# Kernel tuning notes

Measured on AMD Instinct MI355X. Metric: run time of the kernel, lower is better.

Reference implementation:

```python
import jax, jax.numpy as jnp
import numpy as np

DIM = 48
HF = int(DIM * 2.66)  # 127 hidden_features

_DN = ('NCHW', 'OIHW', 'NCHW')

def _gconv3(x, w, groups):
    # 3x3 grouped conv, stride 1, zero pad 1 (torch Conv2d default padding)
    return jax.lax.conv_general_dilated(x, w, (1, 1), [(1, 1), (1, 1)],
                                         dimension_numbers=_DN,
                                         feature_group_count=groups)

def _g1x1(x, w):
    # grouped 1x1 conv; w: (groups, out_per_group, in_per_group)
    B, C, H, W = x.shape
    g = w.shape[0]
    xr = x.reshape(B, g, C // g, H, W)
    y = jnp.einsum('bgihw,goi->bgohw', xr, w)
    return y.reshape(B, g * w.shape[1], H, W)

def _shuffle(x):
    # channel shuffle with 4 groups (reshape/permute as in the torch module)
    B, C, H, W = x.shape
    return x.reshape(B, C // 4, 4, H * W).transpose(0, 2, 1, 3).reshape(B, C, H, W)

def _avgconv(x):
    # frozen dense 3x3 conv with all weights 1/9 and replicate padding:
    # every output channel equals box_blur(sum over input channels) / 9
    s = jnp.sum(x, axis=1, keepdims=True) * jnp.asarray(1.0 / 9.0, x.dtype)
    sp = jnp.pad(s, ((0, 0), (0, 0), (1, 1), (1, 1)), mode='edge')
    k = jnp.ones((1, 1, 3, 3), x.dtype)
    b = jax.lax.conv_general_dilated(sp, k, (1, 1), 'VALID', dimension_numbers=_DN)
    return jnp.broadcast_to(b, x.shape)

def setup_inputs() -> dict:
    key = jax.random.key(0)
    ks = jax.random.split(key, 10)
    s = 0.05
    return {
        'x':     jax.random.normal(ks[0], (2, DIM, 256, 256), jnp.float32),
        'w_inP': jax.random.normal(ks[1], (2 * HF, DIM), jnp.float32) * s,
        'w_inD': jax.random.normal(ks[2], (4 * HF, 1, 3, 3), jnp.float32) * s,
        'w_lp1': jax.random.normal(ks[3], (HF, 4, 4), jnp.float32) * s,
        'w_hp1': jax.random.normal(ks[4], (HF, 4, 4), jnp.float32) * s,
        'w_lp2': jax.random.normal(ks[5], (HF, 4, 4), jnp.float32) * s,
        'w_hp2': jax.random.normal(ks[6], (HF, 4, 4), jnp.float32) * s,
        'w_ld':  jax.random.normal(ks[7], (HF, 4, 3, 3), jnp.float32) * s,
        'w_hd':  jax.random.normal(ks[8], (HF, 4, 3, 3), jnp.float32) * s,
        'w_out': jax.random.normal(ks[9], (DIM, 2 * HF), jnp.float32) * s,
    }

def reference(x, w_inP, w_inD, w_lp1, w_hp1, w_lp2, w_hp2, w_ld, w_hd, w_out):
    residual = x
    # inPconv (dense 1x1) -> inDconv (groups=2h, multiplier 2) -> ReLU
    t = jnp.einsum('bchw,oc->bohw', x, w_inP)            # (B, 2h, H, W)
    t = jax.nn.relu(_gconv3(t, w_inD, 2 * HF))            # (B, 4h, H, W)
    l = _avgconv(t)
    h = t - l
    l = jax.nn.relu(_g1x1(l, w_lp1))
    h = jax.nn.relu(_g1x1(h, w_hp1))
    l = _shuffle(l)
    h = _shuffle(h)
    l2 = _g1x1(l, w_lp2)
    h2 = _g1x1(h, w_hp2)
    c = 2 * HF
    l_tol, l_toh = l2[:, :c], l2[:, c:]
    h_toh, h_tol = h2[:, :c], h2[:, c:]
    l = jax.nn.relu(_gconv3(jnp.concatenate([l_tol, h_tol], axis=1), w_ld, HF))
    h = jax.nn.relu(_gconv3(jnp.concatenate([h_toh, l_toh], axis=1), w_hd, HF))
    out = jnp.einsum('bchw,oc->bohw', jnp.concatenate([l, h], axis=1), w_out)
    return out + residual
```

## Files before the change

kernel.cpp:

```cpp
#include <hip/hip_runtime.h>
#include <hip/hip_bf16.h>

#define HW 65536
#define NCH 16

typedef __attribute__((ext_vector_type(8))) short bf16x8;
typedef __attribute__((ext_vector_type(4))) float f32x4;
typedef __attribute__((ext_vector_type(2))) float f32x2;
typedef __attribute__((ext_vector_type(2))) short s16x2;

__device__ __forceinline__ float bfu(unsigned short u){
    return __uint_as_float(((unsigned int)u) << 16);
}
__device__ __forceinline__ float bflo(unsigned int u){
    return __uint_as_float(u << 16);
}
__device__ __forceinline__ float bfhi(unsigned int u){
    return __uint_as_float(u & 0xffff0000u);
}
__device__ __forceinline__ unsigned short f2bu(float f){
    return __builtin_bit_cast(unsigned short, __float2bfloat16(f));
}
__device__ __forceinline__ unsigned int pk2(float a, float b){
    return (unsigned int)f2bu(a) | ((unsigned int)f2bu(b) << 16);
}
__device__ __forceinline__ unsigned int pk2c(float a, float b){
    unsigned int r;
    asm("v_cvt_pk_bf16_f32 %0, %1, %2" : "=v"(r) : "v"(a), "v"(b));
    return r;
}

#if __has_builtin(__builtin_amdgcn_fdot2_f32_bf16)
__device__ __forceinline__ float DOT2B(s16x2 a, s16x2 b, float c){
    return __builtin_amdgcn_fdot2_f32_bf16(a, b, c, false);
}
#else
__device__ __forceinline__ float DOT2B(s16x2 a, s16x2 b, float c){
    return fmaf(bfu((unsigned short)a.x), bfu((unsigned short)b.x),
           fmaf(bfu((unsigned short)a.y), bfu((unsigned short)b.y), c));
}
#endif

__global__ void k_coef1(const float* __restrict__ wlp1, const float* __restrict__ whp1,
                        const float* __restrict__ wlp2,
                        float* __restrict__ ahp1s,
                        float* __restrict__ cpG, float* __restrict__ cnG){
    __shared__ float aL[508], ah[508];
    int t = threadIdx.x;
    if (t < 508){
        int g = t >> 2, o = t & 3;
        float s = 0.f, s2 = 0.f;
        for (int i = 0; i < 4; ++i){ s += wlp1[g*16 + o*4 + i]; s2 += whp1[g*16 + o*4 + i]; }
        aL[t] = s; ah[t] = s2;
    }
    __syncthreads();
    if (t < 508){
        int g = t >> 2, o = t & 3;
        float p = 0.f, n = 0.f;
        for (int k = 0; k < 4; ++k){
            int idx = 4*g + k;
            int inv = (idx % 127)*4 + idx/127;
            float av = aL[inv];
            float w2 = wlp2[g*16 + o*4 + k];
            p += w2 * fmaxf(av, 0.f);
            n += w2 * fminf(av, 0.f);
        }
        cpG[t] = p; cnG[t] = n;
        int inv = (t % 127)*4 + t/127;
        ahp1s[t] = ah[inv];
    }
}

__global__ void k_coef2(const float* __restrict__ wld, const float* __restrict__ whd,
                        const float* __restrict__ winP, const float* __restrict__ winD,
                        const float* __restrict__ wout,
                        const float* __restrict__ cp, const float* __restrict__ cn,
                        unsigned int* __restrict__ WPNL, unsigned int* __restrict__ WPNH,
                        unsigned int* __restrict__ WLDpk, unsigned int* __restrict__ WHDpk,
                        float* __restrict__ wDp,
                        unsigned short* __restrict__ WPb, unsigned short* __restrict__ BtP){
    int t0 = blockIdx.x*256 + threadIdx.x;
    int str = gridDim.x*256;
    for (int idx = t0; idx < 127*9; idx += str){
        int g = idx/9, q = idx%9;
        float lp=0.f, ln=0.f, hp=0.f, hn=0.f;
        for (int i = 0; i < 4; ++i){
            int ch = 4*g + i;
            if (ch < 254){ float w = wld[g*36 + i*9 + q]; lp += w*cp[ch]; ln += w*cn[ch]; }
            else         { float w = whd[g*36 + i*9 + q]; hp += w*cp[ch]; hn += w*cn[ch]; }
        }
        WPNL[idx] = pk2(lp, ln);
        WPNH[idx] = pk2(hp, hn);
    }
    for (int idx = t0; idx < 127*18; idx += str){
        int g = idx/18, r = idx%18; int q = r >> 1, hp_ = r & 1;
        int c0 = 4*g + 2*hp_, c1 = c0 + 1;
        float wl0 = (c0 >= 254) ? wld[g*36 + (2*hp_)*9 + q]   : 0.f;
        float wl1 = (c1 >= 254) ? wld[g*36 + (2*hp_+1)*9 + q] : 0.f;
        float wh0 = (c0 <  254) ? whd[g*36 + (2*hp_)*9 + q]   : 0.f;
        float wh1 = (c1 <  254) ? whd[g*36 + (2*hp_+1)*9 + q] : 0.f;
        WLDpk[idx] = pk2(wl0, wl1);
        WHDpk[idx] = pk2(wh0, wh1);
    }
    for (int idx = t0; idx < 512*9; idx += str){
        int ch = idx/9, q = idx - ch*9;
        wDp[idx] = (ch < 508) ? winD[ch*9 + q] : 0.f;
    }
    for (int idx = t0; idx < 256*64; idx += str){
        int o = idx >> 6, k = idx & 63;
        float vv = (o < 254 && k < 48) ? winP[o*48 + k] : 0.f;
        WPb[idx] = f2bu(vv);
    }
    for (int idx = t0; idx < 48*256; idx += str){
        int n = idx >> 8, k = idx & 255;
        int g = k >> 1;
        float vv = (g < 127) ? ((k & 1) ? wout[n*254 + 127 + g] : wout[n*254 + g]) : 0.f;
        BtP[idx] = f2bu(vv);
    }
}

__global__ void k_padU(uint4* __restrict__ u, float* __restrict__ Lm, unsigned int* __restrict__ Lpk,
                       int uRp, int lRp, int nbat, int zeroTop, int zeroBot){
    int p = blockIdx.x, t = threadIdx.x;
    int nu = nbat*32;
    if (p < nu){
        uint4* pl = u + (size_t)p*uRp*258;
        uint4 z = make_uint4(0,0,0,0);
        for (int i = t; i < 258; i += 256){ pl[i] = z; pl[(size_t)(uRp-1)*258 + i] = z; }
        for (int r = t; r < uRp; r += 256){ pl[(size_t)r*258] = z; pl[(size_t)r*258 + 257] = z; }
    } else {
        float* pl = Lm + (size_t)(p-nu)*lRp*258;
        unsigned int* pk = Lpk + (size_t)(p-nu)*lRp*258;
        if (zeroTop) for (int i = t; i < 258; i += 256){ pl[i] = 0.f; pk[i] = 0u; }
        if (zeroBot) for (int i = t; i < 258; i += 256){ pl[(size_t)(lRp-1)*258 + i] = 0.f; pk[(size_t)(lRp-1)*258 + i] = 0u; }
        for (int r = t; r < lRp; r += 256){
            pl[(size_t)r*258] = 0.f; pl[(size_t)r*258 + 257] = 0.f;
            pk[(size_t)r*258] = 0u;  pk[(size_t)r*258 + 257] = 0u;
        }
    }
}

__global__ __launch_bounds__(256) void k_pconv(const float* __restrict__ x,
        const unsigned short* __restrict__ WPb, uint4* __restrict__ u,
        int b0, int ur0, int urows, int uRp){
    __shared__ unsigned short BtS[256*72];
    int t = threadIdx.x;
    for (int i = t; i < 256*64; i += 256){
        int o = i >> 6, k = i & 63;
        BtS[o*72 + k] = WPb[i];
    }
    int bpb = urows*4;
    int bi = blockIdx.x / bpb;
    int r  = blockIdx.x - bi*bpb;
    int lr = r >> 2, quarter = r & 3;
    int b = b0 + bi;
    int grow = ur0 + lr;
    const float* xb = x + (size_t)b*48*HW + (size_t)grow*256 + quarter*64;
    int w = t >> 6, lane = t & 63;
    int px = w*16 + (lane & 15);
    int k0 = (lane >> 4)*8;
    bf16x8 afr[2];
    #pragma unroll
    for (int kk = 0; kk < 2; ++kk){
        #pragma unroll
        for (int j = 0; j < 8; ++j){
            int k = kk*32 + k0 + j;
            float vv = (k < 48) ? xb[(size_t)k*HW + px] : 0.f;
            afr[kk][j] = (short)f2bu(vv);
        }
    }
    __syncthreads();
    f32x4 acc[16];
    #pragma unroll
    for (int nt = 0; nt < 16; ++nt) acc[nt] = (f32x4){0.f,0.f,0.f,0.f};
    #pragma unroll
    for (int kk = 0; kk < 2; ++kk){
        #pragma unroll
        for (int nt = 0; nt < 16; ++nt){
            bf16x8 bfr = *reinterpret_cast<const bf16x8*>(&BtS[(nt*16 + (lane&15))*72 + kk*32 + k0]);
            acc[nt] = __builtin_amdgcn_mfma_f32_16x16x32_bf16(afr[kk], bfr, acc[nt], 0, 0, 0);
        }
    }
    __syncthreads();
    unsigned short* E = BtS;
    #pragma unroll
    for (int nt = 0; nt < 16; ++nt){
        #pragma unroll
        for (int rg = 0; rg < 4; ++rg){
            int epx = w*16 + (lane>>4)*4 + rg;
            int eo  = nt*16 + (lane&15);
            E[epx*264 + eo] = f2bu(acc[nt][rg]);
        }
    }
    __syncthreads();
    int spx = t & 63;
    size_t su = (size_t)uRp*258;
    uint4* ub = u + (size_t)bi*32*su + (size_t)(lr+1)*258 + (quarter*64 + spx + 1);
    int og = t >> 6;
    #pragma unroll
    for (int j = 0; j < 8; ++j){
        int od = og*8 + j;
        uint4 q4 = *reinterpret_cast<const uint4*>(&E[spx*264 + od*8]);
        ub[(size_t)od*su] = q4;
    }
}

__global__ __launch_bounds__(256) void k_dw(const uint4* __restrict__ u,
        const float* __restrict__ wDp, const float* __restrict__ whp1,
        unsigned short* __restrict__ d1s, float* __restrict__ Sp,
        int tr0, int trows, int ur0, int uRp, int tR, int nbat){
    int chunk = blockIdx.x & (NCH-1);
    int rb = blockIdx.x >> 4;
    int bi = rb / trows;
    int lr = rb - bi*trows;
    int grow = tr0 + lr;
    int xx = threadIdx.x;
    int lrow = grow - ur0;
    size_t su = (size_t)uRp*258;
    const uint4* ubase = u + (size_t)bi*32*su + (size_t)lrow*258 + xx;
    unsigned short* db = d1s + (size_t)bi*127*tR*256*4 + ((size_t)lr*256 + xx)*4;
    size_t dcs = (size_t)tR*256*4;
    float ssum = 0.f;
    int od0 = chunk*2;
    for (int od = od0; od < od0+2; ++od){
        const uint4* up = ubase + (size_t)od*su;
        float o[16];
        #pragma unroll
        for (int j = 0; j < 16; ++j) o[j] = 0.f;
        #pragma unroll
        for (int q = 0; q < 9; ++q){
            uint4 rv = up[(q/3)*258 + (q%3)];
            float c0 = bflo(rv.x), c1 = bfhi(rv.x), c2 = bflo(rv.y), c3 = bfhi(rv.y);
            float c4 = bflo(rv.z), c5 = bfhi(rv.z), c6 = bflo(rv.w), c7 = bfhi(rv.w);
            const float* wq = wDp + (size_t)(16*od)*9 + q;
            o[0]  = fmaf(wq[0],   c0, o[0]);
            o[1]  = fmaf(wq[9],   c0, o[1]);
            o[2]  = fmaf(wq[18],  c1, o[2]);
            o[3]  = fmaf(wq[27],  c1, o[3]);
            o[4]  = fmaf(wq[36],  c2, o[4]);
            o[5]  = fmaf(wq[45],  c2, o[5]);
            o[6]  = fmaf(wq[54],  c3, o[6]);
            o[7]  = fmaf(wq[63],  c3, o[7]);
            o[8]  = fmaf(wq[72],  c4, o[8]);
            o[9]  = fmaf(wq[81],  c4, o[9]);
            o[10] = fmaf(wq[90],  c5, o[10]);
            o[11] = fmaf(wq[99],  c5, o[11]);
            o[12] = fmaf(wq[108], c6, o[12]);
            o[13] = fmaf(wq[117], c6, o[13]);
            o[14] = fmaf(wq[126], c7, o[14]);
            o[15] = fmaf(wq[135], c7, o[15]);
        }
        #pragma unroll
        for (int j = 0; j < 16; ++j){ o[j] = fmaxf(o[j], 0.f); ssum += o[j]; }
        int tqb = 4*od;
        #pragma unroll
        for (int m = 0; m < 4; ++m){
            int tq = tqb + m;
            if (tq < 127){
                const float* w1 = whp1 + tq*16;
                #pragma unroll
                for (int oi = 0; oi < 4; ++oi){
                    float d = fmaf(w1[oi*4+0], o[4*m+0], fmaf(w1[oi*4+1], o[4*m+1],
                              fmaf(w1[oi*4+2], o[4*m+2], w1[oi*4+3]*o[4*m+3])));
                    int idx = 127*oi + tq;
                    db[(size_t)(idx>>2)*dcs + (idx&3)] = f2bu(d);
                }
            }
        }
    }
    Sp[((size_t)(chunk*nbat + bi)*tR + lr)*256 + xx] = ssum * (1.f/9.f);
}

__global__ __launch_bounds__(256) void k_box(const float* __restrict__ Sp, float* __restrict__ Lm,
        unsigned int* __restrict__ Lpk,
        int lr0, int lrows, int tr0, int tR, int a, int lRp, int nbat){
    int bi = blockIdx.x / lrows;
    int lr = blockIdx.x - bi*lrows;
    int grow = lr0 + lr;
    int xx = threadIdx.x;
    int g0 = (grow-1 > 0 ? grow-1 : 0) - tr0, g1 = grow - tr0, g2 = (grow+1 < 255 ? grow+1 : 255) - tr0;
    int x0 = xx-1 > 0 ? xx-1 : 0, x2 = xx+1 < 255 ? xx+1 : 255;
    float s = 0.f;
    for (int ch = 0; ch < NCH; ++ch){
        const float* Sb = Sp + ((size_t)(ch*nbat + bi)*tR)*256;
        s += Sb[g0*256+x0]+Sb[g0*256+xx]+Sb[g0*256+x2]
           + Sb[g1*256+x0]+Sb[g1*256+xx]+Sb[g1*256+x2]
           + Sb[g2*256+x0]+Sb[g2*256+xx]+Sb[g2*256+x2];
    }
    size_t o = (size_t)bi*lRp*258 + (size_t)(grow-a+1)*258 + xx + 1;
    Lm[o] = s;
    Lpk[o] = pk2c(fmaxf(s, 0.f), fminf(s, 0.f));
}

__global__ __launch_bounds__(256) void k_mov(const ushort4* __restrict__ d1s,
     const float* __restrict__ Lm, const unsigned int* __restrict__ Lpk,
     const float* __restrict__ whp2, const float* __restrict__ ahp1s,
     const unsigned int* __restrict__ WPNL, const unsigned int* __restrict__ WPNH,
     const unsigned int* __restrict__ WLDpk, const unsigned int* __restrict__ WHDpk,
     unsigned int* __restrict__ v,
     int a, int orows, int tr0, int tR, int lRp){
    __shared__ uint2 h2t[10][258];
    int g = blockIdx.x % 127;
    int rest = blockIdx.x / 127;
    int ntiles = orows >> 3;
    int ti = rest % ntiles;
    int bi = rest / ntiles;
    int px = threadIdx.x;
    int row0 = a + ti*8;
    const ushort4* db = d1s + ((size_t)bi*127 + g)*tR*256;
    const float* Lb = Lm + (size_t)bi*lRp*258;
    float as0 = ahp1s[4*g], as1 = ahp1s[4*g+1], as2 = ahp1s[4*g+2], as3 = ahp1s[4*g+3];
    float w2r[16];
    #pragma unroll
    for (int i = 0; i < 16; ++i) w2r[i] = whp2[g*16 + i];
    #pragma unroll
    for (int rr = 0; rr < 10; ++rr){
        int gr = row0 - 1 + rr;
        uint2 hv; hv.x = 0u; hv.y = 0u;
        if (gr >= 0 && gr < 256){
            ushort4 dq = db[(size_t)(gr - tr0)*256 + px];
            float Lv = Lb[(size_t)(gr - a + 1)*258 + px + 1];
            float h0 = fmaxf(fmaf(-Lv, as0, bfu(dq.x)), 0.f);
            float h1 = fmaxf(fmaf(-Lv, as1, bfu(dq.y)), 0.f);
            float hm2 = fmaxf(fmaf(-Lv, as2, bfu(dq.z)), 0.f);
            float h3 = fmaxf(fmaf(-Lv, as3, bfu(dq.w)), 0.f);
            float a0 = fmaf(w2r[0], h0, fmaf(w2r[1], h1, fmaf(w2r[2], hm2, w2r[3]*h3)));
            float a1 = fmaf(w2r[4], h0, fmaf(w2r[5], h1, fmaf(w2r[6], hm2, w2r[7]*h3)));
            float a2 = fmaf(w2r[8], h0, fmaf(w2r[9], h1, fmaf(w2r[10], hm2, w2r[11]*h3)));
            float a3 = fmaf(w2r[12], h0, fmaf(w2r[13], h1, fmaf(w2r[14], hm2, w2r[15]*h3)));
            hv.x = pk2c(a0, a1);
            hv.y = pk2c(a2, a3);
        }
        h2t[rr][px+1] = hv;
    }
    if (px < 10){ uint2 z; z.x = 0u; z.y = 0u; h2t[px][0] = z; h2t[px][257] = z; }
    __syncthreads();
    s16x2 WPl[9], WPh[9];
    #pragma unroll
    for (int q = 0; q < 9; ++q){
        WPl[q] = __builtin_bit_cast(s16x2, WPNL[g*9+q]);
        WPh[q] = __builtin_bit_cast(s16x2, WPNH[g*9+q]);
    }
    bool lbr = (g >= 63), hbr = (g <= 63);
    s16x2 WDl[18], WDh[18];
    #pragma unroll
    for (int i = 0; i < 18; ++i){
        WDl[i] = __builtin_bit_cast(s16x2, WLDpk[g*18+i]);
        WDh[i] = __builtin_bit_cast(s16x2, WHDpk[g*18+i]);
    }
    size_t ps = (size_t)orows*256;
    unsigned int* vb = v + ((size_t)bi*128 + g)*ps + (size_t)(ti*8)*256 + px;
    const unsigned int* Lq = Lpk + (size_t)bi*lRp*258 + (size_t)(ti*8)*258 + px;
    s16x2 lq[3][3];
    uint2 ta[3][3];
    #pragma unroll
    for (int rr = 0; rr < 2; ++rr){
        #pragma unroll
        for (int c = 0; c < 3; ++c){
            lq[rr][c] = __builtin_bit_cast(s16x2, Lq[(size_t)rr*258 + c]);
            ta[rr][c] = h2t[rr][px + c];
        }
    }
    #pragma unroll
    for (int r = 0; r < 8; ++r){
        #pragma unroll
        for (int c = 0; c < 3; ++c){
            lq[2][c] = __builtin_bit_cast(s16x2, Lq[(size_t)(r+2)*258 + c]);
            ta[2][c] = h2t[r+2][px + c];
        }
        float sl0 = 0.f, sl1 = 0.f, sh0 = 0.f, sh1 = 0.f;
        #pragma unroll
        for (int dy = 0; dy < 3; ++dy){
            #pragma unroll
            for (int dx = 0; dx < 3; ++dx){
                int q = dy*3 + dx;
                if (q & 1){ sl1 = DOT2B(lq[dy][dx], WPl[q], sl1); sh1 = DOT2B(lq[dy][dx], WPh[q], sh1); }
                else      { sl0 = DOT2B(lq[dy][dx], WPl[q], sl0); sh0 = DOT2B(lq[dy][dx], WPh[q], sh0); }
            }
        }
        if (lbr){
            #pragma unroll
            for (int dy = 0; dy < 3; ++dy){
                #pragma unroll
                for (int dx = 0; dx < 3; ++dx){
                    int q = dy*3 + dx;
                    uint2 tv = ta[dy][dx];
                    sl0 = DOT2B(__builtin_bit_cast(s16x2, tv.x), WDl[2*q],   sl0);
                    sl1 = DOT2B(__builtin_bit_cast(s16x2, tv.y), WDl[2*q+1], sl1);
                }
            }
        }
        if (hbr){
            #pragma unroll
            for (int dy = 0; dy < 3; ++dy){
                #pragma unroll
                for (int dx = 0; dx < 3; ++dx){
                    int q = dy*3 + dx;
                    uint2 tv = ta[dy][dx];
                    sh0 = DOT2B(__builtin_bit_cast(s16x2, tv.x), WDh[2*q],   sh0);
                    sh1 = DOT2B(__builtin_bit_cast(s16x2, tv.y), WDh[2*q+1], sh1);
                }
            }
        }
        vb[(size_t)r*256] = pk2c(fmaxf(sl0+sl1, 0.f), fmaxf(sh0+sh1, 0.f));
        if (g == 126) vb[(size_t)r*256 + ps] = 0u;
        #pragma unroll
        for (int c = 0; c < 3; ++c){
            ta[0][c] = ta[1][c]; ta[1][c] = ta[2][c];
            lq[0][c] = lq[1][c]; lq[1][c] = lq[2][c];
        }
    }
}

__global__ __launch_bounds__(256) void k_proj(const unsigned int* __restrict__ v,
        const unsigned short* __restrict__ BtP, const float* __restrict__ x,
        float* __restrict__ out, int b0, int a, int orows){
    __shared__ float EoS[256*49];
    unsigned short* Bt = (unsigned short*)EoS;
    int t = threadIdx.x;
    for (int i = t; i < 48*256; i += 256){
        int n = i >> 8, k = i & 255;
        Bt[n*136 + k] = BtP[i];
    }
    int bi = blockIdx.x / orows;
    int lr = blockIdx.x - bi*orows;
    int b = b0 + bi;
    size_t ps = (size_t)orows*256;
    const unsigned int* vb = v + (size_t)bi*128*ps + (size_t)lr*256;
    int lane = t & 63, w = t >> 6;
    int pxl = w*64;
    __syncthreads();
    f32x4 acc[4][3];
    #pragma unroll
    for (int m = 0; m < 4; ++m)
        #pragma unroll
        for (int nt = 0; nt < 3; ++nt) acc[m][nt] = (f32x4){0.f,0.f,0.f,0.f};
    #pragma unroll
    for (int ch = 0; ch < 4; ++ch){
        bf16x8 bfr[3][2];
        #pragma unroll
        for (int nt = 0; nt < 3; ++nt)
            #pragma unroll
            for (int kk = 0; kk < 2; ++kk)
                bfr[nt][kk] = *reinterpret_cast<const bf16x8*>(
                    &Bt[(nt*16 + (lane&15))*136 + ch*64 + kk*32 + (lane>>4)*8]);
        #pragma unroll
        for (int m = 0; m < 4; ++m){
            int px = pxl + m*16 + (lane & 15);
            #pragma unroll
            for (int kk = 0; kk < 2; ++kk){
                int pl0 = ch*32 + kk*16 + (lane>>4)*4;
                unsigned int p0 = vb[(size_t)(pl0+0)*ps + px];
                unsigned int p1 = vb[(size_t)(pl0+1)*ps + px];
                unsigned int p2 = vb[(size_t)(pl0+2)*ps + px];
                unsigned int p3 = vb[(size_t)(pl0+3)*ps + px];
                bf16x8 af;
                af[0]=(short)(p0&0xffff); af[1]=(short)(p0>>16);
                af[2]=(short)(p1&0xffff); af[3]=(short)(p1>>16);
                af[4]=(short)(p2&0xffff); af[5]=(short)(p2>>16);
                af[6]=(short)(p3&0xffff); af[7]=(short)(p3>>16);
                #pragma unroll
                for (int nt = 0; nt < 3; ++nt)
                    acc[m][nt] = __builtin_amdgcn_mfma_f32_16x16x32_bf16(af, bfr[nt][kk], acc[m][nt], 0, 0, 0);
            }
        }
    }
    __syncthreads();
    #pragma unroll
    for (int m = 0; m < 4; ++m){
        #pragma unroll
        for (int nt = 0; nt < 3; ++nt){
            #pragma unroll
            for (int rg = 0; rg < 4; ++rg){
                int epx = pxl + m*16 + (lane>>4)*4 + rg;
                int eo  = nt*16 + (lane&15);
                EoS[epx*49 + eo] = acc[m][nt][rg];
            }
        }
    }
    __syncthreads();
    int grow = a + lr;
    const float* xb = x + (size_t)b*48*HW + (size_t)grow*256 + t;
    float* ob = out + (size_t)b*48*HW + (size_t)grow*256 + t;
    #pragma unroll
    for (int o = 0; o < 48; ++o)
        ob[(size_t)o*HW] = EoS[t*49 + o] + xb[(size_t)o*HW];
}

extern "C" void kernel_launch(void* const* d_in, const int* in_sizes, int n_in,
                              void* d_out, int out_size, void* d_ws, size_t ws_size,
                              hipStream_t stream){
    const float* x    = (const float*)d_in[0];
    const float* winP = (const float*)d_in[1];
    const float* winD = (const float*)d_in[2];
    const float* wlp1 = (const float*)d_in[3];
    const float* whp1 = (const float*)d_in[4];
    const float* wlp2 = (const float*)d_in[5];
    const float* whp2 = (const float*)d_in[6];
    const float* wld  = (const float*)d_in[7];
    const float* whd  = (const float*)d_in[8];
    const float* wout = (const float*)d_in[9];
    float* out = (float*)d_out;

    char* ws = (char*)d_ws;
    size_t off = 0;
    auto alloc = [&](size_t bytes)->char*{
        char* pp = ws + off; off += (bytes + 255) & ~(size_t)255; return pp;
    };
    auto A = [](size_t bytes)->size_t{ return (bytes + 255) & ~(size_t)255; };

    float* ahp1s = (float*)alloc(508*4);
    float* cpG = (float*)alloc(508*4);
    float* cnG = (float*)alloc(508*4);
    unsigned int* WPNL  = (unsigned int*)alloc(127*9*4);
    unsigned int* WPNH  = (unsigned int*)alloc(127*9*4);
    unsigned int* WLDpk = (unsigned int*)alloc(127*18*4);
    unsigned int* WHDpk = (unsigned int*)alloc(127*18*4);
    float* wDp  = (float*)alloc(512*9*4);
    unsigned short* WPb = (unsigned short*)alloc(256*64*2);
    unsigned short* BtP = (unsigned short*)alloc(48*256*2);

    const int cfgs[6][2] = {{256,2},{128,2},{64,2},{64,1},{32,1},{16,1}};
    int Hb = 16, nbat = 1;
    for (int ci = 0; ci < 6; ++ci){
        int hb = cfgs[ci][0], nb = cfgs[ci][1];
        int uRr = hb+6 < 256 ? hb+6 : 256;
        int tRr = hb+4 < 256 ? hb+4 : 256;
        size_t need = off;
        need += A((size_t)nb*32*(uRr+2)*258*16);
        need += A((size_t)nb*127*tRr*256*8);
        need += A((size_t)nb*NCH*tRr*256*4);
        need += A((size_t)nb*(hb+2)*258*4);
        need += A((size_t)nb*(hb+2)*258*4);
        if (need <= ws_size){ Hb = hb; nbat = nb; break; }
    }
    int uR = Hb+6 < 256 ? Hb+6 : 256;
    int tR = Hb+4 < 256 ? Hb+4 : 256;
    int uRp = uR + 2;
    int lRp = Hb + 2;
    uint4* u   = (uint4*)alloc((size_t)nbat*32*uRp*258*16);
    unsigned short* d1s = (unsigned short*)alloc((size_t)nbat*127*tR*256*8);
    float* Sp = (float*)alloc((size_t)nbat*NCH*tR*256*4);
    float* Lm = (float*)alloc((size_t)nbat*lRp*258*4);
    unsigned int* Lpk = (unsigned int*)alloc((size_t)nbat*lRp*258*4);
    unsigned int* v = (unsigned int*)u;

    k_coef1<<<1, 512, 0, stream>>>(wlp1, whp1, wlp2, ahp1s, cpG, cnG);
    k_coef2<<<64, 256, 0, stream>>>(wld, whd, winP, winD, wout, cpG, cnG,
                                    WPNL, WPNH, WLDpk, WHDpk, wDp, WPb, BtP);

    for (int b0 = 0; b0 < 2; b0 += nbat){
        for (int a = 0; a < 256; a += Hb){
            int ur0 = a-3 > 0 ? a-3 : 0;  int ur1 = a+Hb+3 < 256 ? a+Hb+3 : 256;
            int tr0 = a-2 > 0 ? a-2 : 0;  int tr1 = a+Hb+2 < 256 ? a+Hb+2 : 256;
            int lr0 = a-1 > 0 ? a-1 : 0;  int lr1 = a+Hb+1 < 256 ? a+Hb+1 : 256;
            int urows = ur1-ur0, trows = tr1-tr0, lrows = lr1-lr0;
            int orows = (a+Hb < 256 ? a+Hb : 256) - a;
            k_padU<<<nbat*32 + nbat, 256, 0, stream>>>(u, Lm, Lpk, uRp, lRp, nbat,
                                                       a == 0, a + Hb >= 256);
            k_pconv<<<nbat*urows*4, 256, 0, stream>>>(x, WPb, u, b0, ur0, urows, uRp);
            k_dw  <<<nbat*trows*NCH, 256, 0, stream>>>(u, wDp, whp1, d1s, Sp, tr0, trows, ur0, uRp, tR, nbat);
            k_box <<<nbat*lrows, 256, 0, stream>>>(Sp, Lm, Lpk, lr0, lrows, tr0, tR, a, lRp, nbat);
            k_mov <<<nbat*(orows>>3)*127, 256, 0, stream>>>((const ushort4*)d1s, Lm, Lpk, whp2, ahp1s,
                                                            WPNL, WPNH, WLDpk, WHDpk, v,
                                                            a, orows, tr0, tR, lRp);
            k_proj<<<nbat*orows, 256, 0, stream>>>(v, BtP, x, out, b0, a, orows);
        }
    }
}
```

Measured before the change: 175.3 us.

## Store intermediate d1 as planar per-channel bf16 planes and pack depthwise FMAs

The intermediate d1 buffer moves from an interleaved 4-channel ushort4 layout to one bf16 plane per channel, in both the producer k_dw and the consumer k_mov. Each k_dw store now writes a contiguous 2-byte element per lane across the wavefront instead of a strided 2-byte scatter inside 8-byte groups, which should coalesce writes better. k_mov now issues four separate 2-byte loads per pixel instead of one 8-byte load. The k_dw depthwise accumulation is also rewritten with float2 vectors so the compiler can emit packed FMA instructions.

```diff
diff --git a/kernel.cpp b/kernel.cpp
--- a/kernel.cpp
+++ b/kernel.cpp
@@ -218,52 +218,51 @@
     int lrow = grow - ur0;
     size_t su = (size_t)uRp*258;
     const uint4* ubase = u + (size_t)bi*32*su + (size_t)lrow*258 + xx;
-    unsigned short* db = d1s + (size_t)bi*127*tR*256*4 + ((size_t)lr*256 + xx)*4;
-    size_t dcs = (size_t)tR*256*4;
+    size_t ps_d = (size_t)tR*256;
+    unsigned short* dbs = d1s + (size_t)bi*508*ps_d + (size_t)lr*256 + xx;
     float ssum = 0.f;
     int od0 = chunk*2;
     for (int od = od0; od < od0+2; ++od){
         const uint4* up = ubase + (size_t)od*su;
-        float o[16];
-        #pragma unroll
-        for (int j = 0; j < 16; ++j) o[j] = 0.f;
+        f32x2 P[8];
+        #pragma unroll
+        for (int j = 0; j < 8; ++j) P[j] = (f32x2){0.f, 0.f};
         #pragma unroll
         for (int q = 0; q < 9; ++q){
             uint4 rv = up[(q/3)*258 + (q%3)];
-            float c0 = bflo(rv.x), c1 = bfhi(rv.x), c2 = bflo(rv.y), c3 = bfhi(rv.y);
-            float c4 = bflo(rv.z), c5 = bfhi(rv.z), c6 = bflo(rv.w), c7 = bfhi(rv.w);
+            f32x2 d0 = (f32x2){bflo(rv.x), bfhi(rv.x)};
+            f32x2 d1v = (f32x2){bflo(rv.y), bfhi(rv.y)};
+            f32x2 d2 = (f32x2){bflo(rv.z), bfhi(rv.z)};
+            f32x2 d3 = (f32x2){bflo(rv.w), bfhi(rv.w)};
             const float* wq = wDp + (size_t)(16*od)*9 + q;
-            o[0]  = fmaf(wq[0],   c0, o[0]);
-            o[1]  = fmaf(wq[9],   c0, o[1]);
-            o[2]  = fmaf(wq[18],  c1, o[2]);
-            o[3]  = fmaf(wq[27],  c1, o[3]);
-            o[4]  = fmaf(wq[36],  c2, o[4]);
-            o[5]  = fmaf(wq[45],  c2, o[5]);
-            o[6]  = fmaf(wq[54],  c3, o[6]);
-            o[7]  = fmaf(wq[63],  c3, o[7]);
-            o[8]  = fmaf(wq[72],  c4, o[8]);
-            o[9]  = fmaf(wq[81],  c4, o[9]);
-            o[10] = fmaf(wq[90],  c5, o[10]);
-            o[11] = fmaf(wq[99],  c5, o[11]);
-            o[12] = fmaf(wq[108], c6, o[12]);
-            o[13] = fmaf(wq[117], c6, o[13]);
-            o[14] = fmaf(wq[126], c7, o[14]);
-            o[15] = fmaf(wq[135], c7, o[15]);
-        }
-        #pragma unroll
-        for (int j = 0; j < 16; ++j){ o[j] = fmaxf(o[j], 0.f); ssum += o[j]; }
+            P[0] += (f32x2){wq[0],   wq[18]}  * d0;
+            P[1] += (f32x2){wq[9],   wq[27]}  * d0;
+            P[2] += (f32x2){wq[36],  wq[54]}  * d1v;
+            P[3] += (f32x2){wq[45],  wq[63]}  * d1v;
+            P[4] += (f32x2){wq[72],  wq[90]}  * d2;
+            P[5] += (f32x2){wq[81],  wq[99]}  * d2;
+            P[6] += (f32x2){wq[108], wq[126]} * d3;
+            P[7] += (f32x2){wq[117], wq[135]} * d3;
+        }
+        #pragma unroll
+        for (int j = 0; j < 8; ++j){
+            P[j].x = fmaxf(P[j].x, 0.f);
+            P[j].y = fmaxf(P[j].y, 0.f);
+            ssum += P[j].x + P[j].y;
+        }
         int tqb = 4*od;
         #pragma unroll
         for (int m = 0; m < 4; ++m){
             int tq = tqb + m;
             if (tq < 127){
+                float o0 = P[2*m].x, o1 = P[2*m+1].x, o2 = P[2*m].y, o3 = P[2*m+1].y;
                 const float* w1 = whp1 + tq*16;
                 #pragma unroll
                 for (int oi = 0; oi < 4; ++oi){
-                    float d = fmaf(w1[oi*4+0], o[4*m+0], fmaf(w1[oi*4+1], o[4*m+1],
-                              fmaf(w1[oi*4+2], o[4*m+2], w1[oi*4+3]*o[4*m+3])));
+                    float d = fmaf(w1[oi*4+0], o0, fmaf(w1[oi*4+1], o1,
+                              fmaf(w1[oi*4+2], o2, w1[oi*4+3]*o3)));
                     int idx = 127*oi + tq;
-                    db[(size_t)(idx>>2)*dcs + (idx&3)] = f2bu(d);
+                    dbs[(size_t)idx*ps_d] = f2bu(d);
                 }
             }
         }
@@ -292,7 +291,7 @@
     Lpk[o] = pk2c(fmaxf(s, 0.f), fminf(s, 0.f));
 }
 
-__global__ __launch_bounds__(256) void k_mov(const ushort4* __restrict__ d1s,
+__global__ __launch_bounds__(256) void k_mov(const unsigned short* __restrict__ d1s,
      const float* __restrict__ Lm, const unsigned int* __restrict__ Lpk,
      const float* __restrict__ whp2, const float* __restrict__ ahp1s,
      const unsigned int* __restrict__ WPNL, const unsigned int* __restrict__ WPNH,
@@ -307,7 +306,11 @@
     int bi = rest / ntiles;
     int px = threadIdx.x;
     int row0 = a + ti*8;
-    const ushort4* db = d1s + ((size_t)bi*127 + g)*tR*256;
+    size_t ps_d = (size_t)tR*256;
+    const unsigned short* dp0 = d1s + ((size_t)bi*508 + 4*g+0)*ps_d;
+    const unsigned short* dp1 = d1s + ((size_t)bi*508 + 4*g+1)*ps_d;
+    const unsigned short* dp2 = d1s + ((size_t)bi*508 + 4*g+2)*ps_d;
+    const unsigned short* dp3 = d1s + ((size_t)bi*508 + 4*g+3)*ps_d;
     const float* Lb = Lm + (size_t)bi*lRp*258;
     float as0 = ahp1s[4*g], as1 = ahp1s[4*g+1], as2 = ahp1s[4*g+2], as3 = ahp1s[4*g+3];
     float w2r[16];
@@ -318,12 +321,16 @@
         int gr = row0 - 1 + rr;
         uint2 hv; hv.x = 0u; hv.y = 0u;
         if (gr >= 0 && gr < 256){
-            ushort4 dq = db[(size_t)(gr - tr0)*256 + px];
+            size_t ro = (size_t)(gr - tr0)*256 + px;
+            float d0 = bfu(dp0[ro]);
+            float d1 = bfu(dp1[ro]);
+            float d2 = bfu(dp2[ro]);
+            float d3 = bfu(dp3[ro]);
             float Lv = Lb[(size_t)(gr - a + 1)*258 + px + 1];
-            float h0 = fmaxf(fmaf(-Lv, as0, bfu(dq.x)), 0.f);
-            float h1 = fmaxf(fmaf(-Lv, as1, bfu(dq.y)), 0.f);
-            float hm2 = fmaxf(fmaf(-Lv, as2, bfu(dq.z)), 0.f);
-            float h3 = fmaxf(fmaf(-Lv, as3, bfu(dq.w)), 0.f);
+            float h0 = fmaxf(fmaf(-Lv, as0, d0), 0.f);
+            float h1 = fmaxf(fmaf(-Lv, as1, d1), 0.f);
+            float hm2 = fmaxf(fmaf(-Lv, as2, d2), 0.f);
+            float h3 = fmaxf(fmaf(-Lv, as3, d3), 0.f);
             float a0 = fmaf(w2r[0], h0, fmaf(w2r[1], h1, fmaf(w2r[2], hm2, w2r[3]*h3)));
             float a1 = fmaf(w2r[4], h0, fmaf(w2r[5], h1, fmaf(w2r[6], hm2, w2r[7]*h3)));
             float a2 = fmaf(w2r[8], h0, fmaf(w2r[9], h1, fmaf(w2r[10], hm2, w2r[11]*h3)));
@@ -528,7 +535,7 @@
         int tRr = hb+4 < 256 ? hb+4 : 256;
         size_t need = off;
         need += A((size_t)nb*32*(uRr+2)*258*16);
-        need += A((size_t)nb*127*tRr*256*8);
+        need += A((size_t)nb*508*tRr*256*2);
         need += A((size_t)nb*NCH*tRr*256*4);
         need += A((size_t)nb*(hb+2)*258*4);
         need += A((size_t)nb*(hb+2)*258*4);
@@ -539,7 +546,7 @@
     int uRp = uR + 2;
     int lRp = Hb + 2;
     uint4* u   = (uint4*)alloc((size_t)nbat*32*uRp*258*16);
-    unsigned short* d1s = (unsigned short*)alloc((size_t)nbat*127*tR*256*8);
+    unsigned short* d1s = (unsigned short*)alloc((size_t)nbat*508*tR*256*2);
     float* Sp = (float*)alloc((size_t)nbat*NCH*tR*256*4);
     float* Lm = (float*)alloc((size_t)nbat*lRp*258*4);
     unsigned int* Lpk = (unsigned int*)alloc((size_t)nbat*lRp*258*4);
@@ -561,7 +568,7 @@
             k_pconv<<<nbat*urows*4, 256, 0, stream>>>(x, WPb, u, b0, ur0, urows, uRp);
             k_dw  <<<nbat*trows*NCH, 256, 0, stream>>>(u, wDp, whp1, d1s, Sp, tr0, trows, ur0, uRp, tR, nbat);
             k_box <<<nbat*lrows, 256, 0, stream>>>(Sp, Lm, Lpk, lr0, lrows, tr0, tR, a, lRp, nbat);
-            k_mov <<<nbat*(orows>>3)*127, 256, 0, stream>>>((const ushort4*)d1s, Lm, Lpk, whp2, ahp1s,
+            k_mov <<<nbat*(orows>>3)*127, 256, 0, stream>>>(d1s, Lm, Lpk, whp2, ahp1s,
                                                             WPNL, WPNH, WLDpk, WHDpk, v,
                                                             a, orows, tr0, tR, lRp);
             k_proj<<<nbat*orows, 256, 0, stream>>>(v, BtP, x, out, b0, a, orows);
```

After: 162.8 us (median of 2 runs). 7.1% less time.
